# Performance work log

Hardware: AMD Instinct MI355X
Metric: run time of the kernel (lower is better)

The kernel has to match this reference:

```python
import jax, jax.numpy as jnp
import numpy as np

THRESHOLD = 0.5
NEG_POS = 3
ALPHA = 0.5
EPS = 1e-6


def cxcy2xy(b):
    return jnp.concatenate([b[:, :2] - b[:, 2:] / 2, b[:, :2] + b[:, 2:] / 2], axis=1)


def xy2cxcy(b):
    return jnp.concatenate([(b[:, 2:] + b[:, :2]) / 2, b[:, 2:] - b[:, :2]], axis=1)


def encode_boxes(b, d):
    return jnp.concatenate([(b[:, :2] - d[:, :2]) / (d[:, 2:] / 10 + EPS),
                            jnp.log(b[:, 2:] / d[:, 2:] + EPS) * 5], axis=1)


def find_iou(a, b):
    # a: [O,4] xy, b: [N,4] xy -> [O,N]
    lt = jnp.maximum(a[:, None, :2], b[None, :, :2])
    rb = jnp.minimum(a[:, None, 2:], b[None, :, 2:])
    wh = jnp.clip(rb - lt, 0.0)
    inter = wh[..., 0] * wh[..., 1]
    area_a = (a[:, 2] - a[:, 0]) * (a[:, 3] - a[:, 1])
    area_b = (b[:, 2] - b[:, 0]) * (b[:, 3] - b[:, 1])
    return inter / (area_a[:, None] + area_b[None, :] - inter)


def _match(boxes_i, labels_i, def_xy, default_boxes):
    # boxes_i: [O,4] xy, labels_i: [O], def_xy/default_boxes: [N,4]
    n_obj = boxes_i.shape[0]
    overlap = find_iou(boxes_i, def_xy)            # [O, N]
    overlap_defbox = overlap.max(axis=0)           # [N]
    object_defbox = overlap.argmax(axis=0)         # [N]
    defbox_object = overlap.argmax(axis=1)         # [O]
    object_defbox = object_defbox.at[defbox_object].set(jnp.arange(n_obj))
    overlap_defbox = overlap_defbox.at[defbox_object].set(1.0)
    label = labels_i[object_defbox]
    label = jnp.where(overlap_defbox < THRESHOLD, 0, label)
    t_loc = encode_boxes(xy2cxcy(boxes_i[object_defbox]), default_boxes)
    return t_loc, label


def reference(locs_pred, cls_pred, boxes, labels, default_boxes):
    B, N, C = cls_pred.shape
    def_xy = cxcy2xy(default_boxes)
    t_locs, t_classes = jax.vmap(_match, in_axes=(0, 0, None, None))(
        boxes, labels, def_xy, default_boxes)      # [B,N,4], [B,N]

    pos = t_classes != 0                            # [B,N]
    n_pos = pos.sum(axis=1)                         # [B]
    n_pos_total = n_pos.sum().astype(jnp.float32)

    # SmoothL1 (beta=1), mean over positive-box coordinate elements
    d = jnp.abs(locs_pred - t_locs)
    sl1 = jnp.where(d < 1.0, 0.5 * d * d, d - 0.5)
    loc_loss = jnp.sum(sl1 * pos[..., None].astype(sl1.dtype)) / (n_pos_total * 4.0)

    # per-anchor cross entropy
    logp = jax.nn.log_softmax(cls_pred, axis=-1)
    all_conf = -jnp.take_along_axis(logp, t_classes[..., None], axis=-1)[..., 0]  # [B,N]

    pos_conf = jnp.sum(jnp.where(pos, all_conf, 0.0))
    neg_conf = jnp.where(pos, 0.0, all_conf)
    neg_sorted = -jnp.sort(-neg_conf, axis=1)       # descending
    hard = jnp.arange(N)[None, :] < (NEG_POS * n_pos)[:, None]
    hard_sum = jnp.sum(jnp.where(hard, neg_sorted, 0.0))

    conf_loss = (hard_sum + pos_conf) / n_pos_total
    return ALPHA * loc_loss + conf_loss


def setup_inputs() -> dict:
    key = jax.random.key(0)
    k1, k2, k3, k4, k5, k6, k7 = jax.random.split(key, 7)
    B, N, C, O = 32, 24564, 81, 16
    locs_pred = jax.random.normal(k1, (B, N, 4), dtype=jnp.float32)
    cls_pred = jax.random.normal(k2, (B, N, C), dtype=jnp.float32)
    # ground-truth boxes: valid xy boxes inside [0,1]
    cxy = jax.random.uniform(k3, (B, O, 2), minval=0.2, maxval=0.8)
    wh = jax.random.uniform(k4, (B, O, 2), minval=0.05, maxval=0.3)
    boxes = jnp.concatenate([cxy - wh / 2, cxy + wh / 2], axis=-1).astype(jnp.float32)
    labels = jax.random.randint(k5, (B, O), 1, C)
    dcxy = jax.random.uniform(k6, (N, 2), minval=0.05, maxval=0.95)
    dwh = jax.random.uniform(k7, (N, 2), minval=0.05, maxval=0.4)
    default_boxes = jnp.concatenate([dcxy, dwh], axis=-1).astype(jnp.float32)
    return {"locs_pred": locs_pred, "cls_pred": cls_pred, "boxes": boxes,
            "labels": labels, "default_boxes": default_boxes}
```

## Files before the change

### kernel.cpp

```cpp
#include <hip/hip_runtime.h>
#include <math.h>

#define THRESH    0.5f
#define NEG_POSK  3
#define EPSf      1e-6f
#define CCLS      81
#define TILEA     64
#define CHUNKS    16
#define TPB       16

__device__ __forceinline__ float iou_xy(float ax0, float ay0, float ax1, float ay1,
                                        float bx0, float by0, float bx1, float by1) {
    float lx = fmaxf(ax0, bx0), ly = fmaxf(ay0, by0);
    float rx = fminf(ax1, bx1), ry = fminf(ay1, by1);
    float w = fmaxf(rx - lx, 0.f), h = fmaxf(ry - ly, 0.f);
    float inter = w * h;
    float aa = (ax1 - ax0) * (ay1 - ay0);
    float ab = (bx1 - bx0) * (by1 - by0);
    return inter / (aa + ab - inter);
}

__device__ __forceinline__ void gload16(const void* g, void* l) {
    __builtin_amdgcn_global_load_lds(
        (const __attribute__((address_space(1))) void*)g,
        (__attribute__((address_space(3))) void*)l, 16, 0, 0);
}

__global__ __launch_bounds__(256) void k_obj_part(const float* __restrict__ boxes,
                                                  const float* __restrict__ dboxes,
                                                  float* __restrict__ part_iou,
                                                  int* __restrict__ part_idx,
                                                  int N, int O) {
    int bo = blockIdx.x;
    int c  = blockIdx.y;
    const float* bb = boxes + (size_t)bo * 4;
    float ax0 = bb[0], ay0 = bb[1], ax1 = bb[2], ay1 = bb[3];
    int chunk = (N + CHUNKS - 1) / CHUNKS;
    int n0 = c * chunk;
    int n1 = min(n0 + chunk, N);
    float best = -1.f; int bi = 0x7FFFFFFF;
    for (int n = n0 + threadIdx.x; n < n1; n += 256) {
        float4 d = ((const float4*)dboxes)[n];
        float dx0 = d.x - d.z * 0.5f, dy0 = d.y - d.w * 0.5f;
        float dx1 = d.x + d.z * 0.5f, dy1 = d.y + d.w * 0.5f;
        float iou = iou_xy(ax0, ay0, ax1, ay1, dx0, dy0, dx1, dy1);
        if (iou > best) { best = iou; bi = n; }
    }
    #pragma unroll
    for (int dd = 1; dd < 64; dd <<= 1) {
        float v2 = __shfl_xor(best, dd); int i2 = __shfl_xor(bi, dd);
        if (v2 > best || (v2 == best && i2 < bi)) { best = v2; bi = i2; }
    }
    __shared__ float sv[4]; __shared__ int si[4];
    int w = threadIdx.x >> 6;
    if ((threadIdx.x & 63) == 0) { sv[w] = best; si[w] = bi; }
    __syncthreads();
    if (threadIdx.x == 0) {
        #pragma unroll
        for (int i = 1; i < 4; ++i)
            if (sv[i] > best || (sv[i] == best && si[i] < bi)) { best = sv[i]; bi = si[i]; }
        part_iou[(size_t)bo * CHUNKS + c] = best;
        part_idx[(size_t)bo * CHUNKS + c] = bi;
    }
}

__global__ void k_obj_reduce(const float* __restrict__ part_iou,
                             const int* __restrict__ part_idx,
                             int* __restrict__ defbox_object, int BO) {
    int bo = blockIdx.x * blockDim.x + threadIdx.x;
    if (bo >= BO) return;
    float best = -1.f; int bi = 0x7FFFFFFF;
    #pragma unroll
    for (int c = 0; c < CHUNKS; ++c) {
        float v = part_iou[(size_t)bo * CHUNKS + c];
        int  i = part_idx[(size_t)bo * CHUNKS + c];
        if (v > best || (v == best && i < bi)) { best = v; bi = i; }
    }
    defbox_object[bo] = bi;
}

template<int OT>
__global__ __launch_bounds__(256)
void k_conf(const float* __restrict__ locs_pred,
            const float* __restrict__ cls,
            const float* __restrict__ boxes,
            const int* __restrict__ labels,
            const float* __restrict__ dboxes,
            const int* __restrict__ dbo_g,
            float* __restrict__ vneg,
            int* __restrict__ n_pos,
            float* __restrict__ loc_sum,
            float* __restrict__ pos_conf,
            int N, int O_rt, int bpb, int tilesPerBatch) {
    const int O = OT ? OT : O_rt;
    __shared__ __align__(16) float sm[2][TILEA * CCLS];
    __shared__ float sbb[64];
    __shared__ int slab[16], sdbo[16];
    __shared__ float swl[4], swp[4];
    __shared__ int swc[4];
    const int tid = threadIdx.x;
    const int b  = blockIdx.x / bpb;
    const int t0 = (blockIdx.x % bpb) * TPB;
    const int tEnd = min(t0 + TPB, tilesPerBatch);

    if (tid < O * 4) sbb[tid] = boxes[(size_t)b * O * 4 + tid];
    else if (tid < O * 5) slab[tid - O * 4] = labels[(size_t)b * O + tid - O * 4];
    else if (tid < O * 6) sdbo[tid - O * 5] = dbo_g[(size_t)b * O + tid - O * 5];

    const int lane = tid & 63, w = tid >> 6;
    const int j = lane & 15, q = lane >> 4;

    auto stage = [&](int buf, int t) {
        int a0 = t * TILEA;
        int valid = min(TILEA, N - a0);
        const float4* g4 = (const float4*)(cls + ((size_t)b * N + a0) * CCLS);
        float4* s4 = (float4*)sm[buf];
        if (valid == TILEA) {
            #pragma unroll
            for (int k2 = 0; k2 < 5; ++k2) {
                int i4 = w * 64 + k2 * 256;
                gload16(g4 + i4 + lane, s4 + i4);
            }
            if (tid < 16) gload16(g4 + 1280 + tid, s4 + 1280);
        } else {
            int len = valid * CCLS;
            const float* g = (const float*)g4;
            for (int i = tid; i < len; i += 256) sm[buf][i] = g[i];
        }
    };

    stage(0, t0);
    __syncthreads();

    float obx0[4], oby0[4], obx1[4], oby1[4], oarea[4];
    int odbo[4];
    #pragma unroll
    for (int oo = 0; oo < 4; ++oo) {
        int o = q * 4 + oo;
        obx0[oo] = sbb[o*4];   oby0[oo] = sbb[o*4+1];
        obx1[oo] = sbb[o*4+2]; oby1[oo] = sbb[o*4+3];
        oarea[oo] = (obx1[oo] - obx0[oo]) * (oby1[oo] - oby0[oo]);
        odbo[oo] = sdbo[o];
    }

    float pc = 0.f, ls = 0.f; int cnt = 0;

    auto phase2 = [&](int buf, int t) {
        int a0 = t * TILEA;
        int valid = min(TILEA, N - a0);
        int a = w * 16 + j;
        bool act = a < valid;
        int n = a0 + a;
        int nc = min(n, N - 1);
        float4 d = ((const float4*)dboxes)[nc];
        float dx0 = d.x - d.z * 0.5f, dy0 = d.y - d.w * 0.5f;
        float dx1 = d.x + d.z * 0.5f, dy1 = d.y + d.w * 0.5f;
        float areaD = d.z * d.w;
        float bi = -1.f, bu = 1.f; int bsel = q * 4;
        int fs = -1;
        #pragma unroll
        for (int oo = 0; oo < 4; ++oo) {
            float lx = fmaxf(obx0[oo], dx0), ly = fmaxf(oby0[oo], dy0);
            float rx = fminf(obx1[oo], dx1), ry = fminf(oby1[oo], dy1);
            float ww = fmaxf(rx - lx, 0.f), hh = fmaxf(ry - ly, 0.f);
            float inter = ww * hh;
            float uni = oarea[oo] + areaD - inter;
            float c1 = inter * bu, c2 = bi * uni;
            if (c1 > c2) { bi = inter; bu = uni; bsel = q * 4 + oo; }
            if (odbo[oo] == n) fs = q * 4 + oo;
        }
        #pragma unroll
        for (int dd = 16; dd < 64; dd <<= 1) {
            float oi = __shfl_xor(bi, dd), ou = __shfl_xor(bu, dd);
            int os = __shfl_xor(bsel, dd);
            int of = __shfl_xor(fs, dd);
            float c1 = oi * bu, c2 = bi * ou;
            if (c1 > c2 || (c1 == c2 && os < bsel)) { bi = oi; bu = ou; bsel = os; }
            fs = max(fs, of);
        }
        const float* row = &sm[buf][a * CCLS];
        float s = 0.f;
        if (act) {
            int c0 = q * 20;
            #pragma unroll
            for (int i = 0; i < 20; ++i) s += __expf(row[c0 + i]);
            if (q == 3) s += __expf(row[80]);
        }
        s += __shfl_xor(s, 16);
        s += __shfl_xor(s, 32);
        if (act && q == 0) {
            bool forced = fs >= 0;
            int sel = forced ? fs : bsel;
            bool meets = forced || (bi >= 0.5f * bu);
            int lbl = meets ? slab[sel] : 0;
            float conf = __logf(s) - row[lbl];
            bool pos = (lbl != 0);
            size_t idx = (size_t)b * N + n;
            vneg[idx] = pos ? 0.f : conf;
            if (pos) {
                pc += conf; cnt++;
                float bx0 = sbb[sel*4], by0 = sbb[sel*4+1];
                float bx1 = sbb[sel*4+2], by1 = sbb[sel*4+3];
                float bcx = (bx0 + bx1) * 0.5f, bcy = (by0 + by1) * 0.5f;
                float bw = bx1 - bx0, bh = by1 - by0;
                float t0f = (bcx - d.x) / (d.z / 10.0f + EPSf);
                float t1f = (bcy - d.y) / (d.w / 10.0f + EPSf);
                float t2f = __logf(bw / d.z + EPSf) * 5.0f;
                float t3f = __logf(bh / d.w + EPSf) * 5.0f;
                float4 p = ((const float4*)locs_pred)[idx];
                float dd;
                dd = fabsf(p.x - t0f); ls += (dd < 1.f) ? 0.5f*dd*dd : dd - 0.5f;
                dd = fabsf(p.y - t1f); ls += (dd < 1.f) ? 0.5f*dd*dd : dd - 0.5f;
                dd = fabsf(p.z - t2f); ls += (dd < 1.f) ? 0.5f*dd*dd : dd - 0.5f;
                dd = fabsf(p.w - t3f); ls += (dd < 1.f) ? 0.5f*dd*dd : dd - 0.5f;
            }
        }
    };

    int cur = 0;
    for (int t = t0; t < tEnd; ++t) {
        if (t + 1 < tEnd) stage(cur ^ 1, t + 1);
        phase2(cur, t);
        __syncthreads();
        cur ^= 1;
    }

    #pragma unroll
    for (int dd = 1; dd < 64; dd <<= 1) {
        pc  += __shfl_xor(pc, dd);
        ls  += __shfl_xor(ls, dd);
        cnt += __shfl_xor(cnt, dd);
    }
    if (lane == 0) { swp[w] = pc; swl[w] = ls; swc[w] = cnt; }
    __syncthreads();
    if (tid == 0) {
        float P = swp[0] + swp[1] + swp[2] + swp[3];
        float L = swl[0] + swl[1] + swl[2] + swl[3];
        int   C = swc[0] + swc[1] + swc[2] + swc[3];
        if (C) {
            atomicAdd(&n_pos[b], C);
            atomicAdd(loc_sum, L);
            atomicAdd(pos_conf, P);
        }
    }
}

__device__ void wave_select(const int* hist, int nbins, int k, int* out_bin, int* out_k) {
    int lane = threadIdx.x & 63;
    int cum = 0;
    for (int c = nbins / 64 - 1; c >= 0; --c) {
        int val = hist[c * 64 + lane];
        int s = val;
        for (int d = 1; d < 64; d <<= 1) {
            int t = __shfl_down(s, d);
            if (lane + d < 64) s += t;
        }
        int total = __shfl(s, 0);
        if (cum + total >= k) {
            unsigned long long mask = __ballot(cum + s >= k);
            int bl = 63 - __builtin_clzll(mask);
            int sB = __shfl(s, bl);
            int vB = __shfl(val, bl);
            if (lane == 0) {
                *out_bin = c * 64 + bl;
                *out_k = k - (cum + sB - vB);
            }
            return;
        }
        cum += total;
    }
    if (lane == 0) { *out_bin = 0; *out_k = 1; }
}

__global__ __launch_bounds__(1024) void k_select(const float* __restrict__ vneg,
                                                 const int* __restrict__ n_pos,
                                                 float* __restrict__ hard_sum,
                                                 int B, int N) {
    int b = blockIdx.x;
    const float* v = vneg + (size_t)b * N;
    __shared__ int hist[2048];
    __shared__ int bcast_bin, bcast_k;
    __shared__ float swv[16];
    __shared__ int swc[16];
    int np = n_pos[b];
    long long kk = (long long)NEG_POSK * np;
    if (kk > N) kk = N;
    int k = (int)kk;
    if (k <= 0) return;
    int tid = threadIdx.x;

    for (int i = tid; i < 2048; i += 1024) hist[i] = 0;
    __syncthreads();
    for (int n = tid; n < N; n += 1024) {
        unsigned u = __float_as_uint(v[n]);
        atomicAdd(&hist[u >> 20], 1);
    }
    __syncthreads();
    if (tid < 64) wave_select(hist, 2048, k, &bcast_bin, &bcast_k);
    __syncthreads();
    int B1 = bcast_bin, k2 = bcast_k;

    for (int i = tid; i < 2048; i += 1024) hist[i] = 0;
    __syncthreads();
    for (int n = tid; n < N; n += 1024) {
        unsigned u = __float_as_uint(v[n]);
        if ((int)(u >> 20) == B1) atomicAdd(&hist[(u >> 9) & 0x7FF], 1);
    }
    __syncthreads();
    if (tid < 64) wave_select(hist, 2048, k2, &bcast_bin, &bcast_k);
    __syncthreads();
    int B2 = bcast_bin, k3 = bcast_k;
    unsigned pre = ((unsigned)B1 << 11) | (unsigned)B2;

    for (int i = tid; i < 512; i += 1024) hist[i] = 0;
    __syncthreads();
    for (int n = tid; n < N; n += 1024) {
        unsigned u = __float_as_uint(v[n]);
        if ((u >> 9) == pre) atomicAdd(&hist[u & 0x1FF], 1);
    }
    __syncthreads();
    if (tid < 64) wave_select(hist, 512, k3, &bcast_bin, &bcast_k);
    __syncthreads();
    unsigned tau_bits = (pre << 9) | (unsigned)bcast_bin;
    float tau = __uint_as_float(tau_bits);

    float ssum = 0.f; int scnt = 0;
    for (int n = tid; n < N; n += 1024) {
        float x = v[n];
        if (x > tau) { ssum += x; scnt++; }
    }
    for (int d = 1; d < 64; d <<= 1) {
        ssum += __shfl_xor(ssum, d);
        scnt += __shfl_xor(scnt, d);
    }
    int w = tid >> 6;
    if ((tid & 63) == 0) { swv[w] = ssum; swc[w] = scnt; }
    __syncthreads();
    if (tid == 0) {
        float S = 0.f; int Ct = 0;
        for (int i = 0; i < 16; ++i) { S += swv[i]; Ct += swc[i]; }
        float hb = S + (float)(k - Ct) * tau;
        atomicAdd(hard_sum, hb);
    }
}

__global__ void k_final(const int* __restrict__ n_pos,
                        const float* __restrict__ loc_sum,
                        const float* __restrict__ pos_conf,
                        const float* __restrict__ hard_sum,
                        float* __restrict__ out, int B) {
    if (threadIdx.x == 0 && blockIdx.x == 0) {
        int tot = 0;
        for (int b = 0; b < B; ++b) tot += n_pos[b];
        float np = (float)tot;
        float loc = *loc_sum / (np * 4.0f);
        float conf = (*hard_sum + *pos_conf) / np;
        out[0] = 0.5f * loc + conf;
    }
}

extern "C" void kernel_launch(void* const* d_in, const int* in_sizes, int n_in,
                              void* d_out, int out_size, void* d_ws, size_t ws_size,
                              hipStream_t stream) {
    const float* locs_pred = (const float*)d_in[0];
    const float* cls_pred  = (const float*)d_in[1];
    const float* boxes     = (const float*)d_in[2];
    const int*   labels    = (const int*)d_in[3];
    const float* dboxes    = (const float*)d_in[4];

    int N = in_sizes[4] / 4;
    int B = in_sizes[0] / (4 * N);
    int O = in_sizes[3] / B;
    int BO = B * O;

    size_t BN = (size_t)B * N;
    char* ws = (char*)d_ws;
    int*   n_pos    = (int*)ws;
    float* loc_sum  = (float*)(ws + 128);
    float* pos_conf = (float*)(ws + 132);
    float* hard_sum = (float*)(ws + 136);
    float* vneg     = (float*)(ws + 256);
    int*   defbox_object = (int*)(ws + 256 + BN * 4);
    float* part_iou = (float*)(ws + 256 + BN * 4 + (size_t)BO * 4);
    int*   part_idx = (int*)(part_iou + (size_t)BO * CHUNKS);

    hipMemsetAsync(ws, 0, 256, stream);

    dim3 gop(BO, CHUNKS);
    k_obj_part<<<gop, 256, 0, stream>>>(boxes, dboxes, part_iou, part_idx, N, O);
    k_obj_reduce<<<(BO + 255) / 256, 256, 0, stream>>>(part_iou, part_idx,
                                                       defbox_object, BO);
    int tilesPerBatch = (N + TILEA - 1) / TILEA;
    int bpb = (tilesPerBatch + TPB - 1) / TPB;
    dim3 gc(B * bpb);
    if (O == 16)
        k_conf<16><<<gc, 256, 0, stream>>>(locs_pred, cls_pred, boxes, labels, dboxes,
                                           defbox_object, vneg, n_pos, loc_sum,
                                           pos_conf, N, O, bpb, tilesPerBatch);
    else
        k_conf<0><<<gc, 256, 0, stream>>>(locs_pred, cls_pred, boxes, labels, dboxes,
                                          defbox_object, vneg, n_pos, loc_sum,
                                          pos_conf, N, O, bpb, tilesPerBatch);
    k_select<<<B, 1024, 0, stream>>>(vneg, n_pos, hard_sum, B, N);
    k_final<<<1, 1, 0, stream>>>(n_pos, loc_sum, pos_conf, hard_sum, (float*)d_out, B);
}
```

Before: 127.9 us.

## Give each wavefront private LDS staging and replace block barrier with vmcnt waits

```diff
diff --git a/kernel.cpp b/kernel.cpp
--- a/kernel.cpp
+++ b/kernel.cpp
@@ -91,9 +91,9 @@
             int* __restrict__ n_pos,
             float* __restrict__ loc_sum,
             float* __restrict__ pos_conf,
-            int N, int O_rt, int bpb, int tilesPerBatch) {
+            int N, int O_rt, int bpb, int tilesPerBatch, long long maxF4) {
     const int O = OT ? OT : O_rt;
-    __shared__ __align__(16) float sm[2][TILEA * CCLS];
+    __shared__ __align__(16) float sm[4][2][16 * CCLS];
     __shared__ float sbb[64];
     __shared__ int slab[16], sdbo[16];
     __shared__ float swl[4], swp[4];
@@ -111,21 +111,20 @@
     const int j = lane & 15, q = lane >> 4;
 
     auto stage = [&](int buf, int t) {
-        int a0 = t * TILEA;
-        int valid = min(TILEA, N - a0);
-        const float4* g4 = (const float4*)(cls + ((size_t)b * N + a0) * CCLS);
-        float4* s4 = (float4*)sm[buf];
-        if (valid == TILEA) {
-            #pragma unroll
-            for (int k2 = 0; k2 < 5; ++k2) {
-                int i4 = w * 64 + k2 * 256;
-                gload16(g4 + i4 + lane, s4 + i4);
-            }
-            if (tid < 16) gload16(g4 + 1280 + tid, s4 + 1280);
-        } else {
-            int len = valid * CCLS;
-            const float* g = (const float*)g4;
-            for (int i = tid; i < len; i += 256) sm[buf][i] = g[i];
+        long long base4 = (((long long)b * N + (long long)t * TILEA + w * 16)
+                           * CCLS) >> 2;
+        const float4* g4 = (const float4*)cls;
+        float4* s4 = (float4*)&sm[w][buf][0];
+        #pragma unroll
+        for (int k2 = 0; k2 < 5; ++k2) {
+            long long gi = base4 + k2 * 64 + lane;
+            if (gi > maxF4) gi = maxF4;
+            gload16(g4 + gi, s4 + k2 * 64);
+        }
+        if (lane < 4) {
+            long long gi = base4 + 320 + lane;
+            if (gi > maxF4) gi = maxF4;
+            gload16(g4 + gi, s4 + 320);
         }
     };
 
@@ -178,7 +177,7 @@
             if (c1 > c2 || (c1 == c2 && os < bsel)) { bi = oi; bu = ou; bsel = os; }
             fs = max(fs, of);
         }
-        const float* row = &sm[buf][a * CCLS];
+        const float* row = &sm[w][buf][j * CCLS];
         float s = 0.f;
         if (act) {
             int c0 = q * 20;
@@ -196,6 +195,7 @@
             float conf = __logf(s) - row[lbl];
             bool pos = (lbl != 0);
             size_t idx = (size_t)b * N + n;
+            float4 p = ((const float4*)locs_pred)[idx];
             vneg[idx] = pos ? 0.f : conf;
             if (pos) {
                 pc += conf; cnt++;
@@ -207,7 +207,6 @@
                 float t1f = (bcy - d.y) / (d.w / 10.0f + EPSf);
                 float t2f = __logf(bw / d.z + EPSf) * 5.0f;
                 float t3f = __logf(bh / d.w + EPSf) * 5.0f;
-                float4 p = ((const float4*)locs_pred)[idx];
                 float dd;
                 dd = fabsf(p.x - t0f); ls += (dd < 1.f) ? 0.5f*dd*dd : dd - 0.5f;
                 dd = fabsf(p.y - t1f); ls += (dd < 1.f) ? 0.5f*dd*dd : dd - 0.5f;
@@ -219,9 +218,15 @@
 
     int cur = 0;
     for (int t = t0; t < tEnd; ++t) {
-        if (t + 1 < tEnd) stage(cur ^ 1, t + 1);
+        bool has_next = (t + 1 < tEnd);
+        if (has_next) stage(cur ^ 1, t + 1);
+        if (t == t0)
+            asm volatile("s_waitcnt vmcnt(6)" ::: "memory");
+        else if (has_next)
+            asm volatile("s_waitcnt vmcnt(9)" ::: "memory");
+        else
+            asm volatile("s_waitcnt vmcnt(3)" ::: "memory");
         phase2(cur, t);
-        __syncthreads();
         cur ^= 1;
     }
 
@@ -392,15 +397,16 @@
                                                        defbox_object, BO);
     int tilesPerBatch = (N + TILEA - 1) / TILEA;
     int bpb = (tilesPerBatch + TPB - 1) / TPB;
+    long long maxF4 = (((long long)B * N * CCLS) >> 2) - 1;
     dim3 gc(B * bpb);
     if (O == 16)
         k_conf<16><<<gc, 256, 0, stream>>>(locs_pred, cls_pred, boxes, labels, dboxes,
                                            defbox_object, vneg, n_pos, loc_sum,
-                                           pos_conf, N, O, bpb, tilesPerBatch);
+                                           pos_conf, N, O, bpb, tilesPerBatch, maxF4);
     else
         k_conf<0><<<gc, 256, 0, stream>>>(locs_pred, cls_pred, boxes, labels, dboxes,
                                           defbox_object, vneg, n_pos, loc_sum,
-                                          pos_conf, N, O, bpb, tilesPerBatch);
+                                          pos_conf, N, O, bpb, tilesPerBatch, maxF4);
     k_select<<<B, 1024, 0, stream>>>(vneg, n_pos, hard_sum, B, N);
     k_final<<<1, 1, 0, stream>>>(n_pos, loc_sum, pos_conf, hard_sum, (float*)d_out, B);
 }
```

Result: faster. 124.1 us (-3.0%).
